# Kernel tuning notes

Hardware: AMD Instinct MI355X
Metric: run time of the kernel (lower is better)

Reference implementation:

```python
import jax, jax.numpy as jnp
import numpy as np
from math import sqrt

B, LQ, LKV = 4, 1024, 1024
QD = KD = VD = 1024
MODEL_DIM = 1024
H = 16
HD = MODEL_DIM // H  # per-head model_dim = 64


def setup_inputs() -> dict:
    key = jax.random.key(0)
    ks = jax.random.split(key, 10)
    s = 0.02
    return {
        "queries": jax.random.normal(ks[0], (B, LQ, QD), jnp.float32),
        "context": jax.random.normal(ks[1], (B, LKV, KD), jnp.float32),
        # stacked per-head linear weights (torch Linear: y = x @ W.T + b); store as [H, in, out]
        "Wq": jax.random.normal(ks[2], (H, QD, HD), jnp.float32) * s,
        "bq": jax.random.normal(ks[3], (H, HD), jnp.float32) * s,
        "Wk": jax.random.normal(ks[4], (KD, HD * 1 * H), jnp.float32).reshape(H, KD, HD) * s,
        "bk": jax.random.normal(ks[5], (H, HD), jnp.float32) * s,
        "Wv": jax.random.normal(ks[6], (H, VD, HD), jnp.float32) * s,
        "bv": jax.random.normal(ks[7], (H, HD), jnp.float32) * s,
        "Wo": jax.random.normal(ks[8], (H * HD, MODEL_DIM), jnp.float32) * s,
        "bo": jax.random.normal(ks[9], (MODEL_DIM,), jnp.float32) * s,
    }


def reference(queries, context, Wq, bq, Wk, bk, Wv, bv, Wo, bo):
    # queries: [B,Lq,Dq]; context: [B,Lkv,Dk]
    # Per-head projections, batched over heads (equivalent to the torch per-head loop).
    q = jnp.einsum("bld,hdm->bhlm", queries, Wq) + bq[None, :, None, :]  # [B,H,Lq,hd]
    k = jnp.einsum("bld,hdm->bhlm", context, Wk) + bk[None, :, None, :]  # [B,H,Lkv,hd]
    v = jnp.einsum("bld,hdm->bhlm", context, Wv) + bv[None, :, None, :]  # [B,H,Lkv,hd]

    scale = 1.0 / sqrt(HD)
    scores = jnp.einsum("bhqd,bhkd->bhqk", q, k) * scale  # [B,H,Lq,Lkv]
    att = jax.nn.softmax(scores, axis=-1)
    head_out = jnp.einsum("bhqk,bhkd->bhqd", att, v)  # [B,H,Lq,hd]

    # torch concatenates heads along the last dim in head order 0..H-1
    multi = head_out.transpose(0, 2, 1, 3).reshape(B, LQ, H * HD)
    residual = q.transpose(0, 2, 1, 3).reshape(B, LQ, H * HD)

    out = multi @ Wo + bo  # [B,Lq,model_dim]
    return out, residual
```

## Files before the change

### kernel.cpp

```cpp
#include <hip/hip_runtime.h>
#include <hip/hip_bf16.h>


typedef unsigned short u16;
typedef __attribute__((ext_vector_type(8))) short short8;
typedef __attribute__((ext_vector_type(4))) float f32x4;

__device__ __forceinline__ float bf2f(u16 u) {
    union { unsigned int i; float f; } c;
    c.i = ((unsigned int)u) << 16;
    return c.f;
}

__device__ __forceinline__ u16 f2bf(float f) {
    unsigned int x = __float_as_uint(f);
    unsigned int r = (x + 0x7fffu + ((x >> 16) & 1u)) >> 16;
    return (u16)r;
}

__device__ __forceinline__ void glds16(u16* lds, const u16* g) {
    __builtin_amdgcn_global_load_lds(
        (const __attribute__((address_space(1))) void*)g,
        (__attribute__((address_space(3))) void*)lds, 16, 0, 0);
}

__global__ __launch_bounds__(256) void prep(
    const float* __restrict__ q, const float* __restrict__ ctx,
    const float* __restrict__ Wq, const float* __restrict__ Wk,
    const float* __restrict__ Wv, const float* __restrict__ Wo,
    u16* __restrict__ Aq, u16* __restrict__ Ac,
    u16* __restrict__ Wqt, u16* __restrict__ Wkt,
    u16* __restrict__ Wvt, u16* __restrict__ Wot)
{
    __shared__ float ls[64][65];
    const int t = threadIdx.x;
    int bid = blockIdx.x;

    if (bid < 4096) {
        const float* in = (bid < 2048) ? q : ctx;
        u16* out = (bid < 2048) ? Aq : Ac;
        size_t i = ((size_t)(bid & 2047) * 256 + t) * 8;
        float4 v0 = *(const float4*)(in + i);
        float4 v1 = *(const float4*)(in + i + 4);
        short8 p;
        p[0] = (short)f2bf(v0.x); p[1] = (short)f2bf(v0.y);
        p[2] = (short)f2bf(v0.z); p[3] = (short)f2bf(v0.w);
        p[4] = (short)f2bf(v1.x); p[5] = (short)f2bf(v1.y);
        p[6] = (short)f2bf(v1.z); p[7] = (short)f2bf(v1.w);
        *(short8*)(out + i) = p;
        return;
    }
    bid -= 4096;
    const float* in; u16* out; int C; size_t moff; int rt, ct;
    if (bid < 768) {
        const int m = bid >> 8, idx = bid & 255;
        in = (m == 0) ? Wq : (m == 1) ? Wk : Wv;
        out = (m == 0) ? Wqt : (m == 1) ? Wkt : Wvt;
        C = 64; rt = (idx & 15) * 64; ct = 0; moff = (size_t)(idx >> 4) * 65536;
    } else {
        const int idx = bid - 768;
        in = Wo; out = Wot; C = 1024; moff = 0;
        rt = (idx & 15) * 64; ct = (idx >> 4) * 64;
    }
    #pragma unroll
    for (int i = 0; i < 4; ++i) {
        int s = i * 256 + t;
        int row = s >> 4, chunk = s & 15;
        float4 v = *(const float4*)(in + moff + (size_t)(rt + row) * C + ct + chunk * 4);
        ls[row][chunk * 4 + 0] = v.x;
        ls[row][chunk * 4 + 1] = v.y;
        ls[row][chunk * 4 + 2] = v.z;
        ls[row][chunk * 4 + 3] = v.w;
    }
    __syncthreads();
    #pragma unroll
    for (int i = 0; i < 2; ++i) {
        int s = i * 256 + t;
        int n = s >> 3, kc = s & 7;
        short8 p;
        #pragma unroll
        for (int j = 0; j < 8; ++j) p[j] = (short)f2bf(ls[kc * 8 + j][n]);
        *(short8*)(out + moff + (size_t)(ct + n) * 1024 + rt + kc * 8) = p;
    }
}

__global__ __launch_bounds__(256, 2) void gemm_qkv(
    const u16* __restrict__ Aq, const u16* __restrict__ Ac,
    const u16* __restrict__ Wqt, const u16* __restrict__ Wkt,
    const u16* __restrict__ Wvt,
    const float* __restrict__ bq, const float* __restrict__ bk,
    const float* __restrict__ bv,
    u16* __restrict__ qws, u16* __restrict__ kws, u16* __restrict__ vtws,
    float* __restrict__ resid)
{
    __shared__ u16 As[128 * 32];
    __shared__ u16 B1[128 * 32];
    __shared__ u16 B2[128 * 32];
    const int n0 = blockIdx.x * 128, m0 = blockIdx.y * 128, z = blockIdx.z;
    const int t = threadIdx.x;
    const int w = t >> 6, lane = t & 63;
    const int quad = lane >> 4, c = lane & 15;
    const int srow = w * 32 + (lane >> 2);
    const int sch = lane & 3;

    u16* lA = As + w * 32 * 32;
    u16* lB1 = B1 + w * 32 * 32;
    u16* lB2 = B2 + w * 32 * 32;
    const u16* afr = As + ((w >> 1) * 64 + c) * 32 + quad * 8;
    const u16* b1fr = B1 + ((w & 1) * 64 + c) * 32 + quad * 8;
    const u16* b2fr = B2 + ((w & 1) * 64 + c) * 32 + quad * 8;
    const int h = blockIdx.x * 2 + (w & 1);

    if (z == 0) {
        const u16* gA = Aq + (size_t)(m0 + srow) * 1024 + sch * 8;
        const u16* gB = Wqt + (size_t)(n0 + srow) * 1024 + sch * 8;
        f32x4 acc[4][4] = {};
        for (int kt = 0; kt < 1024; kt += 32) {
            glds16(lA,           gA + kt);
            glds16(lA + 16 * 32, gA + kt + 16 * 1024);
            glds16(lB1,           gB + kt);
            glds16(lB1 + 16 * 32, gB + kt + 16 * 1024);
            __syncthreads();
            short8 af[4], bf[4];
            #pragma unroll
            for (int rs = 0; rs < 4; ++rs) af[rs] = *(const short8*)(afr + rs * 16 * 32);
            #pragma unroll
            for (int cs = 0; cs < 4; ++cs) bf[cs] = *(const short8*)(b1fr + cs * 16 * 32);
            #pragma unroll
            for (int rs = 0; rs < 4; ++rs)
                #pragma unroll
                for (int cs = 0; cs < 4; ++cs)
                    acc[rs][cs] = __builtin_amdgcn_mfma_f32_16x16x32_bf16(
                        af[rs], bf[cs], acc[rs][cs], 0, 0, 0);
            __syncthreads();
        }
        float bb[4];
        #pragma unroll
        for (int cs = 0; cs < 4; ++cs) bb[cs] = bq[h * 64 + cs * 16 + c];
        #pragma unroll
        for (int rs = 0; rs < 4; ++rs)
            #pragma unroll
            for (int r = 0; r < 4; ++r) {
                const int row = m0 + (w >> 1) * 64 + rs * 16 + quad * 4 + r;
                const int b = row >> 10, l = row & 1023;
                u16* drow = qws + (((size_t)(b * 16 + h) * 1024) + l) * 64;
                float* rrow = resid + (size_t)row * 1024 + h * 64;
                #pragma unroll
                for (int cs = 0; cs < 4; ++cs) {
                    float v = acc[rs][cs][r] + bb[cs];
                    drow[cs * 16 + c] = f2bf(v * 0.125f);
                    rrow[cs * 16 + c] = v;
                }
            }
    } else {
        const u16* gA = Ac + (size_t)(m0 + srow) * 1024 + sch * 8;
        const u16* gBk = Wkt + (size_t)(n0 + srow) * 1024 + sch * 8;
        const u16* gBv = Wvt + (size_t)(n0 + srow) * 1024 + sch * 8;
        f32x4 acck[4][4] = {};
        f32x4 accv[4][4] = {};
        for (int kt = 0; kt < 1024; kt += 32) {
            glds16(lA,            gA + kt);
            glds16(lA + 16 * 32,  gA + kt + 16 * 1024);
            glds16(lB1,           gBk + kt);
            glds16(lB1 + 16 * 32, gBk + kt + 16 * 1024);
            glds16(lB2,           gBv + kt);
            glds16(lB2 + 16 * 32, gBv + kt + 16 * 1024);
            __syncthreads();
            short8 af[4], bkf[4], bvf[4];
            #pragma unroll
            for (int rs = 0; rs < 4; ++rs) af[rs] = *(const short8*)(afr + rs * 16 * 32);
            #pragma unroll
            for (int cs = 0; cs < 4; ++cs) {
                bkf[cs] = *(const short8*)(b1fr + cs * 16 * 32);
                bvf[cs] = *(const short8*)(b2fr + cs * 16 * 32);
            }
            #pragma unroll
            for (int rs = 0; rs < 4; ++rs)
                #pragma unroll
                for (int cs = 0; cs < 4; ++cs) {
                    acck[rs][cs] = __builtin_amdgcn_mfma_f32_16x16x32_bf16(
                        af[rs], bkf[cs], acck[rs][cs], 0, 0, 0);
                    accv[rs][cs] = __builtin_amdgcn_mfma_f32_16x16x32_bf16(
                        af[rs], bvf[cs], accv[rs][cs], 0, 0, 0);
                }
            __syncthreads();
        }
        float bbk[4], bbv[4];
        #pragma unroll
        for (int cs = 0; cs < 4; ++cs) {
            bbk[cs] = bk[h * 64 + cs * 16 + c];
            bbv[cs] = bv[h * 64 + cs * 16 + c];
        }
        #pragma unroll
        for (int rs = 0; rs < 4; ++rs) {
            #pragma unroll
            for (int r = 0; r < 4; ++r) {
                const int row = m0 + (w >> 1) * 64 + rs * 16 + quad * 4 + r;
                const int b = row >> 10, l = row & 1023;
                u16* drow = kws + (((size_t)(b * 16 + h) * 1024) + l) * 64;
                #pragma unroll
                for (int cs = 0; cs < 4; ++cs)
                    drow[cs * 16 + c] = f2bf(acck[rs][cs][r] + bbk[cs]);
            }
            const int l0 = m0 + (w >> 1) * 64 + rs * 16 + quad * 4;
            const int b = l0 >> 10, l = l0 & 1023;
            #pragma unroll
            for (int cs = 0; cs < 4; ++cs) {
                const int hd = cs * 16 + c;
                ushort4 pk;
                pk.x = f2bf(accv[rs][cs][0] + bbv[cs]);
                pk.y = f2bf(accv[rs][cs][1] + bbv[cs]);
                pk.z = f2bf(accv[rs][cs][2] + bbv[cs]);
                pk.w = f2bf(accv[rs][cs][3] + bbv[cs]);
                *(ushort4*)(vtws + ((size_t)(b * 16 + h) * 64 + hd) * 1024 + l) = pk;
            }
        }
    }
}

__global__ __launch_bounds__(256, 3) void gemm_out(
    const u16* __restrict__ A, const u16* __restrict__ Wot,
    const float* __restrict__ bo, float* __restrict__ out)
{
    __shared__ u16 As[128 * 32];
    __shared__ u16 Bs[64 * 32];
    const int f = blockIdx.x;
    const int xcd = f & 7, k = f >> 3;
    const int m0 = (xcd * 4 + (k & 3)) * 128;
    const int n0 = (k >> 2) * 64;
    const int t = threadIdx.x;
    const int w = t >> 6, lane = t & 63;
    const int quad = lane >> 4, c = lane & 15;

    const int arow = w * 32 + (lane >> 2), ach = lane & 3;
    const int brow = w * 16 + (lane >> 2);
    const u16* gA = A + (size_t)(m0 + arow) * 1024 + ach * 8;
    const u16* gB = Wot + (size_t)(n0 + brow) * 1024 + ach * 8;
    u16* lA = As + w * 32 * 32;
    u16* lB = Bs + w * 16 * 32;
    const u16* afr = As + ((w >> 1) * 64 + c) * 32 + quad * 8;
    const u16* bfr = Bs + ((w & 1) * 32 + c) * 32 + quad * 8;

    f32x4 acc[4][2] = {};
    for (int kt = 0; kt < 1024; kt += 32) {
        glds16(lA,           gA + kt);
        glds16(lA + 16 * 32, gA + kt + 16 * 1024);
        glds16(lB,           gB + kt);
        __syncthreads();
        short8 af[4], bf[2];
        #pragma unroll
        for (int rs = 0; rs < 4; ++rs) af[rs] = *(const short8*)(afr + rs * 16 * 32);
        #pragma unroll
        for (int cs = 0; cs < 2; ++cs) bf[cs] = *(const short8*)(bfr + cs * 16 * 32);
        #pragma unroll
        for (int rs = 0; rs < 4; ++rs)
            #pragma unroll
            for (int cs = 0; cs < 2; ++cs)
                acc[rs][cs] = __builtin_amdgcn_mfma_f32_16x16x32_bf16(
                    af[rs], bf[cs], acc[rs][cs], 0, 0, 0);
        __syncthreads();
    }

    const int nb = n0 + (w & 1) * 32;
    float bb[2];
    #pragma unroll
    for (int cs = 0; cs < 2; ++cs) bb[cs] = bo[nb + cs * 16 + c];

    #pragma unroll
    for (int rs = 0; rs < 4; ++rs) {
        #pragma unroll
        for (int r = 0; r < 4; ++r) {
            const int row = m0 + (w >> 1) * 64 + rs * 16 + quad * 4 + r;
            float* orow = out + (size_t)row * 1024 + nb;
            #pragma unroll
            for (int cs = 0; cs < 2; ++cs)
                orow[cs * 16 + c] = acc[rs][cs][r] + bb[cs];
        }
    }
}

__global__ __launch_bounds__(256, 4) void attn_mfma(
    const u16* __restrict__ qws, const u16* __restrict__ kws,
    const u16* __restrict__ vtws, u16* __restrict__ multi)
{
    __shared__ u16 Ks[64 * 64];
    __shared__ u16 Vs[64 * 64];
    __shared__ u16 Ps[4][16 * 72];
    const int t = threadIdx.x;
    const int wave = t >> 6, lane = t & 63;
    const int quad = lane >> 4, c = lane & 15;
    const int bh = blockIdx.y, b = bh >> 4, h = bh & 15;
    const int q0 = blockIdx.x * 64 + wave * 16;

    const u16* qb = qws + ((size_t)bh * 1024 + q0) * 64;
    const u16* kb = kws + (size_t)bh * 65536;
    const u16* vb = vtws + (size_t)bh * 65536;

    short8 qa0 = *(const short8*)(qb + (size_t)c * 64 + quad * 8);
    short8 qa1 = *(const short8*)(qb + (size_t)c * 64 + 32 + quad * 8);

    const int srow = wave * 16 + (lane >> 3);
    const int gch = (lane & 7) ^ ((lane >> 3) & 7);
    u16* ldsK0 = Ks + (wave * 16) * 64;
    u16* ldsK1 = Ks + (wave * 16 + 8) * 64;
    u16* ldsV0 = Vs + (wave * 16) * 64;
    u16* ldsV1 = Vs + (wave * 16 + 8) * 64;
    const u16* gK0 = kb + (size_t)srow * 64 + gch * 8;
    const u16* gK1 = kb + (size_t)(srow + 8) * 64 + gch * 8;
    const u16* gV0 = vb + (size_t)srow * 1024 + gch * 8;
    const u16* gV1 = vb + (size_t)(srow + 8) * 1024 + gch * 8;

    f32x4 O[4] = {};
    float ps[4] = {0.f, 0.f, 0.f, 0.f};
    u16* pw = &Ps[wave][0];
    const int cx = c & 7;

    for (int kt = 0; kt < 1024; kt += 64) {
        glds16(ldsK0, gK0 + (size_t)kt * 64);
        glds16(ldsK1, gK1 + (size_t)kt * 64);
        glds16(ldsV0, gV0 + kt);
        glds16(ldsV1, gV1 + kt);
        __syncthreads();

        f32x4 s[4];
        #pragma unroll
        for (int nt = 0; nt < 4; ++nt) {
            const u16* kr = Ks + (nt * 16 + c) * 64;
            short8 kb0 = *(const short8*)(kr + ((quad ^ cx)) * 8);
            short8 kb1 = *(const short8*)(kr + (((4 + quad) ^ cx)) * 8);
            f32x4 z = {};
            z = __builtin_amdgcn_mfma_f32_16x16x32_bf16(qa0, kb0, z, 0, 0, 0);
            z = __builtin_amdgcn_mfma_f32_16x16x32_bf16(qa1, kb1, z, 0, 0, 0);
            s[nt] = z;
        }

        #pragma unroll
        for (int nt = 0; nt < 4; ++nt)
            #pragma unroll
            for (int r = 0; r < 4; ++r) {
                float p = __expf(s[nt][r]);
                ps[r] += p;
                pw[(quad * 4 + r) * 72 + nt * 16 + c] = (u16)(__float_as_uint(p) >> 16);
            }
        short8 pa0 = *(const short8*)(pw + c * 72 + quad * 8);
        short8 pa1 = *(const short8*)(pw + c * 72 + 32 + quad * 8);

        #pragma unroll
        for (int nt = 0; nt < 4; ++nt) {
            const u16* vr = Vs + (nt * 16 + c) * 64;
            short8 vb0 = *(const short8*)(vr + ((quad ^ cx)) * 8);
            short8 vb1 = *(const short8*)(vr + (((4 + quad) ^ cx)) * 8);
            O[nt] = __builtin_amdgcn_mfma_f32_16x16x32_bf16(pa0, vb0, O[nt], 0, 0, 0);
            O[nt] = __builtin_amdgcn_mfma_f32_16x16x32_bf16(pa1, vb1, O[nt], 0, 0, 0);
        }
        __syncthreads();
    }

    float inv[4];
    #pragma unroll
    for (int r = 0; r < 4; ++r) {
        float sum = ps[r];
        sum += __shfl_xor(sum, 1);
        sum += __shfl_xor(sum, 2);
        sum += __shfl_xor(sum, 4);
        sum += __shfl_xor(sum, 8);
        inv[r] = 1.0f / sum;
    }

    u16* ob = multi + ((size_t)b * 1024 + q0 + quad * 4) * 1024 + h * 64 + c;
    #pragma unroll
    for (int r = 0; r < 4; ++r) {
        u16* orow = ob + (size_t)r * 1024;
        orow[0]  = f2bf(O[0][r] * inv[r]);
        orow[16] = f2bf(O[1][r] * inv[r]);
        orow[32] = f2bf(O[2][r] * inv[r]);
        orow[48] = f2bf(O[3][r] * inv[r]);
    }
}

extern "C" void kernel_launch(void* const* d_in, const int* in_sizes, int n_in,
                              void* d_out, int out_size, void* d_ws, size_t ws_size,
                              hipStream_t stream) {
    const float* queries = (const float*)d_in[0];
    const float* context = (const float*)d_in[1];
    const float* Wq = (const float*)d_in[2];
    const float* bq = (const float*)d_in[3];
    const float* Wk = (const float*)d_in[4];
    const float* bk = (const float*)d_in[5];
    const float* Wv = (const float*)d_in[6];
    const float* bv = (const float*)d_in[7];
    const float* Wo = (const float*)d_in[8];
    const float* bo = (const float*)d_in[9];

    float* out = (float*)d_out;
    float* resid = out + (size_t)4 * 1024 * 1024;

    const size_t M1 = 1024 * 1024;
    u16* Aq   = (u16*)d_ws;
    u16* Ac   = Aq + 4 * M1;
    u16* Wqt  = Ac + 4 * M1;
    u16* Wkt  = Wqt + M1;
    u16* Wvt  = Wkt + M1;
    u16* Wot  = Wvt + M1;
    u16* qws  = Wot + M1;
    u16* kws  = qws + 4 * M1;
    u16* vtws = kws + 4 * M1;
    u16* mws  = vtws + 4 * M1;

    prep<<<5120, 256, 0, stream>>>(queries, context, Wq, Wk, Wv, Wo,
                                   Aq, Ac, Wqt, Wkt, Wvt, Wot);
    gemm_qkv<<<dim3(8, 32, 2), 256, 0, stream>>>(Aq, Ac, Wqt, Wkt, Wvt,
                                                 bq, bk, bv, qws, kws, vtws, resid);
    attn_mfma<<<dim3(16, 64), 256, 0, stream>>>(qws, kws, vtws, mws);
    gemm_out<<<512, 256, 0, stream>>>(mws, Wot, bo, out);
}
```

Baseline: 202.1 us.

## Widen GEMM K-tile with swizzled LDS, split QKV grid, move residual write to attention

Both GEMMs now stage 64-wide K tiles into XOR-swizzled LDS, which halves the number of barriers per K sweep and targets bank conflicts. The fused K/V branch is replaced by a uniform per-z projection over three z-slices, which lowers register pressure and raises block count. The fp32 residual store moves from the Q GEMM epilogue into the attention kernel, reconstructed from the bf16 scaled q, so the residual loses precision. Attention blocks are remapped so each XCD handles contiguous heads for L2 locality, and occupancy hints in launch bounds are dropped.

```diff
diff --git a/kernel.cpp b/kernel.cpp
--- a/kernel.cpp
+++ b/kernel.cpp
@@ -84,146 +84,107 @@
     }
 }
 
-__global__ __launch_bounds__(256, 2) void gemm_qkv(
+__global__ __launch_bounds__(256) void gemm_qkv(
     const u16* __restrict__ Aq, const u16* __restrict__ Ac,
     const u16* __restrict__ Wqt, const u16* __restrict__ Wkt,
     const u16* __restrict__ Wvt,
     const float* __restrict__ bq, const float* __restrict__ bk,
     const float* __restrict__ bv,
-    u16* __restrict__ qws, u16* __restrict__ kws, u16* __restrict__ vtws,
-    float* __restrict__ resid)
+    u16* __restrict__ qws, u16* __restrict__ kws, u16* __restrict__ vtws)
 {
-    __shared__ u16 As[128 * 32];
-    __shared__ u16 B1[128 * 32];
-    __shared__ u16 B2[128 * 32];
+    __shared__ u16 As[128 * 64];
+    __shared__ u16 Bs[128 * 64];
     const int n0 = blockIdx.x * 128, m0 = blockIdx.y * 128, z = blockIdx.z;
     const int t = threadIdx.x;
     const int w = t >> 6, lane = t & 63;
     const int quad = lane >> 4, c = lane & 15;
-    const int srow = w * 32 + (lane >> 2);
-    const int sch = lane & 3;
-
-    u16* lA = As + w * 32 * 32;
-    u16* lB1 = B1 + w * 32 * 32;
-    u16* lB2 = B2 + w * 32 * 32;
-    const u16* afr = As + ((w >> 1) * 64 + c) * 32 + quad * 8;
-    const u16* b1fr = B1 + ((w & 1) * 64 + c) * 32 + quad * 8;
-    const u16* b2fr = B2 + ((w & 1) * 64 + c) * 32 + quad * 8;
-    const int h = blockIdx.x * 2 + (w & 1);
-
-    if (z == 0) {
-        const u16* gA = Aq + (size_t)(m0 + srow) * 1024 + sch * 8;
-        const u16* gB = Wqt + (size_t)(n0 + srow) * 1024 + sch * 8;
-        f32x4 acc[4][4] = {};
-        for (int kt = 0; kt < 1024; kt += 32) {
-            glds16(lA,           gA + kt);
-            glds16(lA + 16 * 32, gA + kt + 16 * 1024);
-            glds16(lB1,           gB + kt);
-            glds16(lB1 + 16 * 32, gB + kt + 16 * 1024);
-            __syncthreads();
+    const int cx = c & 7;
+
+    const u16* A = (z == 0) ? Aq : Ac;
+    const u16* Wt = ((z == 0) ? Wqt : (z == 1) ? Wkt : Wvt) + (size_t)n0 * 1024;
+    const float* bias = (z == 0) ? bq : (z == 1) ? bk : bv;
+
+    const int sr = w * 8 + (lane >> 3);
+    const int gch = (lane & 7) ^ ((lane >> 3) & 7);
+    const u16* gA = A + (size_t)(m0 + sr) * 1024 + gch * 8;
+    const u16* gB = Wt + (size_t)sr * 1024 + gch * 8;
+
+    const int arow = (w >> 1) * 64 + c;
+    const int brow = (w & 1) * 64 + c;
+
+    f32x4 acc[4][4] = {};
+
+    for (int kt = 0; kt < 1024; kt += 64) {
+        #pragma unroll
+        for (int i = 0; i < 4; ++i) {
+            glds16(As + (i * 32 + w * 8) * 64, gA + (size_t)i * 32 * 1024 + kt);
+            glds16(Bs + (i * 32 + w * 8) * 64, gB + (size_t)i * 32 * 1024 + kt);
+        }
+        __syncthreads();
+        #pragma unroll
+        for (int kh = 0; kh < 2; ++kh) {
+            const int ch = (kh * 4 + quad);
             short8 af[4], bf[4];
             #pragma unroll
-            for (int rs = 0; rs < 4; ++rs) af[rs] = *(const short8*)(afr + rs * 16 * 32);
-            #pragma unroll
-            for (int cs = 0; cs < 4; ++cs) bf[cs] = *(const short8*)(b1fr + cs * 16 * 32);
+            for (int rs = 0; rs < 4; ++rs)
+                af[rs] = *(const short8*)(As + (arow + rs * 16) * 64 + (ch ^ cx) * 8);
+            #pragma unroll
+            for (int cs = 0; cs < 4; ++cs)
+                bf[cs] = *(const short8*)(Bs + (brow + cs * 16) * 64 + (ch ^ cx) * 8);
             #pragma unroll
             for (int rs = 0; rs < 4; ++rs)
                 #pragma unroll
                 for (int cs = 0; cs < 4; ++cs)
                     acc[rs][cs] = __builtin_amdgcn_mfma_f32_16x16x32_bf16(
                         af[rs], bf[cs], acc[rs][cs], 0, 0, 0);
-            __syncthreads();
-        }
-        float bb[4];
-        #pragma unroll
-        for (int cs = 0; cs < 4; ++cs) bb[cs] = bq[h * 64 + cs * 16 + c];
+        }
+        __syncthreads();
+    }
+
+    const int h = blockIdx.x * 2 + (w & 1);
+    float bb[4];
+    #pragma unroll
+    for (int cs = 0; cs < 4; ++cs) bb[cs] = bias[h * 64 + cs * 16 + c];
+
+    if (z == 2) {
+        #pragma unroll
+        for (int rs = 0; rs < 4; ++rs) {
+            const int l0 = m0 + (w >> 1) * 64 + rs * 16 + quad * 4;
+            const int b = l0 >> 10, l = l0 & 1023;
+            #pragma unroll
+            for (int cs = 0; cs < 4; ++cs) {
+                const int hd = cs * 16 + c;
+                ushort4 pk;
+                pk.x = f2bf(acc[rs][cs][0] + bb[cs]);
+                pk.y = f2bf(acc[rs][cs][1] + bb[cs]);
+                pk.z = f2bf(acc[rs][cs][2] + bb[cs]);
+                pk.w = f2bf(acc[rs][cs][3] + bb[cs]);
+                *(ushort4*)(vtws + ((size_t)(b * 16 + h) * 64 + hd) * 1024 + l) = pk;
+            }
+        }
+    } else {
+        u16* dst = (z == 0) ? qws : kws;
+        const float scale = (z == 0) ? 0.125f : 1.0f;
         #pragma unroll
         for (int rs = 0; rs < 4; ++rs)
             #pragma unroll
             for (int r = 0; r < 4; ++r) {
                 const int row = m0 + (w >> 1) * 64 + rs * 16 + quad * 4 + r;
                 const int b = row >> 10, l = row & 1023;
-                u16* drow = qws + (((size_t)(b * 16 + h) * 1024) + l) * 64;
-                float* rrow = resid + (size_t)row * 1024 + h * 64;
-                #pragma unroll
-                for (int cs = 0; cs < 4; ++cs) {
-                    float v = acc[rs][cs][r] + bb[cs];
-                    drow[cs * 16 + c] = f2bf(v * 0.125f);
-                    rrow[cs * 16 + c] = v;
-                }
-            }
-    } else {
-        const u16* gA = Ac + (size_t)(m0 + srow) * 1024 + sch * 8;
-        const u16* gBk = Wkt + (size_t)(n0 + srow) * 1024 + sch * 8;
-        const u16* gBv = Wvt + (size_t)(n0 + srow) * 1024 + sch * 8;
-        f32x4 acck[4][4] = {};
-        f32x4 accv[4][4] = {};
-        for (int kt = 0; kt < 1024; kt += 32) {
-            glds16(lA,            gA + kt);
-            glds16(lA + 16 * 32,  gA + kt + 16 * 1024);
-            glds16(lB1,           gBk + kt);
-            glds16(lB1 + 16 * 32, gBk + kt + 16 * 1024);
-            glds16(lB2,           gBv + kt);
-            glds16(lB2 + 16 * 32, gBv + kt + 16 * 1024);
-            __syncthreads();
-            short8 af[4], bkf[4], bvf[4];
-            #pragma unroll
-            for (int rs = 0; rs < 4; ++rs) af[rs] = *(const short8*)(afr + rs * 16 * 32);
-            #pragma unroll
-            for (int cs = 0; cs < 4; ++cs) {
-                bkf[cs] = *(const short8*)(b1fr + cs * 16 * 32);
-                bvf[cs] = *(const short8*)(b2fr + cs * 16 * 32);
-            }
-            #pragma unroll
-            for (int rs = 0; rs < 4; ++rs)
-                #pragma unroll
-                for (int cs = 0; cs < 4; ++cs) {
-                    acck[rs][cs] = __builtin_amdgcn_mfma_f32_16x16x32_bf16(
-                        af[rs], bkf[cs], acck[rs][cs], 0, 0, 0);
-                    accv[rs][cs] = __builtin_amdgcn_mfma_f32_16x16x32_bf16(
-                        af[rs], bvf[cs], accv[rs][cs], 0, 0, 0);
-                }
-            __syncthreads();
-        }
-        float bbk[4], bbv[4];
-        #pragma unroll
-        for (int cs = 0; cs < 4; ++cs) {
-            bbk[cs] = bk[h * 64 + cs * 16 + c];
-            bbv[cs] = bv[h * 64 + cs * 16 + c];
-        }
-        #pragma unroll
-        for (int rs = 0; rs < 4; ++rs) {
-            #pragma unroll
-            for (int r = 0; r < 4; ++r) {
-                const int row = m0 + (w >> 1) * 64 + rs * 16 + quad * 4 + r;
-                const int b = row >> 10, l = row & 1023;
-                u16* drow = kws + (((size_t)(b * 16 + h) * 1024) + l) * 64;
+                u16* drow = dst + (((size_t)(b * 16 + h) * 1024) + l) * 64;
                 #pragma unroll
                 for (int cs = 0; cs < 4; ++cs)
-                    drow[cs * 16 + c] = f2bf(acck[rs][cs][r] + bbk[cs]);
+                    drow[cs * 16 + c] = f2bf((acc[rs][cs][r] + bb[cs]) * scale);
             }
-            const int l0 = m0 + (w >> 1) * 64 + rs * 16 + quad * 4;
-            const int b = l0 >> 10, l = l0 & 1023;
-            #pragma unroll
-            for (int cs = 0; cs < 4; ++cs) {
-                const int hd = cs * 16 + c;
-                ushort4 pk;
-                pk.x = f2bf(accv[rs][cs][0] + bbv[cs]);
-                pk.y = f2bf(accv[rs][cs][1] + bbv[cs]);
-                pk.z = f2bf(accv[rs][cs][2] + bbv[cs]);
-                pk.w = f2bf(accv[rs][cs][3] + bbv[cs]);
-                *(ushort4*)(vtws + ((size_t)(b * 16 + h) * 64 + hd) * 1024 + l) = pk;
-            }
-        }
-    }
-}
-
-__global__ __launch_bounds__(256, 3) void gemm_out(
+    }
+}
+
+__global__ __launch_bounds__(256) void gemm_out(
     const u16* __restrict__ A, const u16* __restrict__ Wot,
     const float* __restrict__ bo, float* __restrict__ out)
 {
-    __shared__ u16 As[128 * 32];
-    __shared__ u16 Bs[64 * 32];
+    __shared__ u16 As[128 * 64];
+    __shared__ u16 Bs[64 * 64];
     const int f = blockIdx.x;
     const int xcd = f & 7, k = f >> 3;
     const int m0 = (xcd * 4 + (k & 3)) * 128;
@@ -231,33 +192,42 @@
     const int t = threadIdx.x;
     const int w = t >> 6, lane = t & 63;
     const int quad = lane >> 4, c = lane & 15;
-
-    const int arow = w * 32 + (lane >> 2), ach = lane & 3;
-    const int brow = w * 16 + (lane >> 2);
-    const u16* gA = A + (size_t)(m0 + arow) * 1024 + ach * 8;
-    const u16* gB = Wot + (size_t)(n0 + brow) * 1024 + ach * 8;
-    u16* lA = As + w * 32 * 32;
-    u16* lB = Bs + w * 16 * 32;
-    const u16* afr = As + ((w >> 1) * 64 + c) * 32 + quad * 8;
-    const u16* bfr = Bs + ((w & 1) * 32 + c) * 32 + quad * 8;
+    const int cx = c & 7;
+
+    const int sr = w * 8 + (lane >> 3);
+    const int gch = (lane & 7) ^ ((lane >> 3) & 7);
+    const u16* gA = A + (size_t)(m0 + sr) * 1024 + gch * 8;
+    const u16* gB = Wot + (size_t)(n0 + sr) * 1024 + gch * 8;
+
+    const int arow = (w >> 1) * 64 + c;
+    const int brow = (w & 1) * 32 + c;
 
     f32x4 acc[4][2] = {};
-    for (int kt = 0; kt < 1024; kt += 32) {
-        glds16(lA,           gA + kt);
-        glds16(lA + 16 * 32, gA + kt + 16 * 1024);
-        glds16(lB,           gB + kt);
-        __syncthreads();
-        short8 af[4], bf[2];
-        #pragma unroll
-        for (int rs = 0; rs < 4; ++rs) af[rs] = *(const short8*)(afr + rs * 16 * 32);
-        #pragma unroll
-        for (int cs = 0; cs < 2; ++cs) bf[cs] = *(const short8*)(bfr + cs * 16 * 32);
-        #pragma unroll
-        for (int rs = 0; rs < 4; ++rs)
+    for (int kt = 0; kt < 1024; kt += 64) {
+        #pragma unroll
+        for (int i = 0; i < 4; ++i)
+            glds16(As + (i * 32 + w * 8) * 64, gA + (size_t)i * 32 * 1024 + kt);
+        #pragma unroll
+        for (int i = 0; i < 2; ++i)
+            glds16(Bs + (i * 32 + w * 8) * 64, gB + (size_t)i * 32 * 1024 + kt);
+        __syncthreads();
+        #pragma unroll
+        for (int kh = 0; kh < 2; ++kh) {
+            const int ch = (kh * 4 + quad);
+            short8 af[4], bf[2];
+            #pragma unroll
+            for (int rs = 0; rs < 4; ++rs)
+                af[rs] = *(const short8*)(As + (arow + rs * 16) * 64 + (ch ^ cx) * 8);
             #pragma unroll
             for (int cs = 0; cs < 2; ++cs)
-                acc[rs][cs] = __builtin_amdgcn_mfma_f32_16x16x32_bf16(
-                    af[rs], bf[cs], acc[rs][cs], 0, 0, 0);
+                bf[cs] = *(const short8*)(Bs + (brow + cs * 16) * 64 + (ch ^ cx) * 8);
+            #pragma unroll
+            for (int rs = 0; rs < 4; ++rs)
+                #pragma unroll
+                for (int cs = 0; cs < 2; ++cs)
+                    acc[rs][cs] = __builtin_amdgcn_mfma_f32_16x16x32_bf16(
+                        af[rs], bf[cs], acc[rs][cs], 0, 0, 0);
+        }
         __syncthreads();
     }
 
@@ -279,9 +249,10 @@
     }
 }
 
-__global__ __launch_bounds__(256, 4) void attn_mfma(
+__global__ __launch_bounds__(256) void attn_mfma(
     const u16* __restrict__ qws, const u16* __restrict__ kws,
-    const u16* __restrict__ vtws, u16* __restrict__ multi)
+    const u16* __restrict__ vtws, u16* __restrict__ multi,
+    float* __restrict__ resid)
 {
     __shared__ u16 Ks[64 * 64];
     __shared__ u16 Vs[64 * 64];
@@ -289,8 +260,12 @@
     const int t = threadIdx.x;
     const int wave = t >> 6, lane = t & 63;
     const int quad = lane >> 4, c = lane & 15;
-    const int bh = blockIdx.y, b = bh >> 4, h = bh & 15;
-    const int q0 = blockIdx.x * 64 + wave * 16;
+    const int f = blockIdx.x;
+    const int xcd = f & 7, j = f >> 3;
+    const int bh = xcd * 8 + (j & 7);
+    const int qt = j >> 3;
+    const int b = bh >> 4, h = bh & 15;
+    const int q0 = qt * 64 + wave * 16;
 
     const u16* qb = qws + ((size_t)bh * 1024 + q0) * 64;
     const u16* kb = kws + (size_t)bh * 65536;
@@ -375,6 +350,13 @@
         orow[16] = f2bf(O[1][r] * inv[r]);
         orow[32] = f2bf(O[2][r] * inv[r]);
         orow[48] = f2bf(O[3][r] * inv[r]);
+    }
+
+    float* rr = resid + ((size_t)b * 1024 + q0 + c) * 1024 + h * 64;
+    #pragma unroll
+    for (int jj = 0; jj < 8; ++jj) {
+        rr[quad * 8 + jj]      = bf2f((u16)qa0[jj]) * 8.0f;
+        rr[32 + quad * 8 + jj] = bf2f((u16)qa1[jj]) * 8.0f;
     }
 }
 
@@ -409,8 +391,8 @@
 
     prep<<<5120, 256, 0, stream>>>(queries, context, Wq, Wk, Wv, Wo,
                                    Aq, Ac, Wqt, Wkt, Wvt, Wot);
-    gemm_qkv<<<dim3(8, 32, 2), 256, 0, stream>>>(Aq, Ac, Wqt, Wkt, Wvt,
-                                                 bq, bk, bv, qws, kws, vtws, resid);
-    attn_mfma<<<dim3(16, 64), 256, 0, stream>>>(qws, kws, vtws, mws);
+    gemm_qkv<<<dim3(8, 32, 3), 256, 0, stream>>>(Aq, Ac, Wqt, Wkt, Wvt,
+                                                 bq, bk, bv, qws, kws, vtws);
+    attn_mfma<<<1024, 256, 0, stream>>>(qws, kws, vtws, mws, resid);
     gemm_out<<<512, 256, 0, stream>>>(mws, Wot, bo, out);
 }
```

After: 201.5 us. Within noise of the previous version (-0.3%).
